# Performance work log

Hardware: AMD Instinct MI355X
Metric: run time of the kernel (lower is better)

Reference implementation:

```python
import jax, jax.numpy as jnp
import numpy as np

DN = ('NCHW', 'OIHW', 'NCHW')

def _conv(x, w, b):
    y = jax.lax.conv_general_dilated(x, w, (1, 1), 'SAME', dimension_numbers=DN)
    return y + b[None, :, None, None]

def _prelu(x, a):
    return jnp.where(x >= 0, x, a * x)

def _block(x, W1, b1, a1, W2, b2, a2, W3, b3):
    x = _prelu(_conv(x, W1, b1), a1)
    x = _prelu(_conv(x, W2, b2), a2)
    return _conv(x, W3, b3)

def setup_inputs() -> dict:
    key = jax.random.key(0)
    B, n_ions, n_primal, H, W = 1, 1, 5, 96, 96
    A, D, n_iter = 96, 96, 10
    P, X = H * W, n_ions * D
    ks = jax.random.split(key, 12)
    f = jax.random.normal
    return {
        'dual': f(ks[0], (B, n_ions, A, D), jnp.float32),
        'primal': f(ks[1], (B, n_primal, H, W, 1), jnp.float32),
        'projection': f(ks[2], (B, n_ions, A, D), jnp.float32),
        'S': f(ks[3], (A, B, P, X), jnp.float32) * 0.01,
        'S_norm': f(ks[4], (A, B, P, X), jnp.float32) * 0.01,
        'dW1': f(ks[5], (n_iter, 32, 3 * n_ions, 3, 3), jnp.float32) * 0.05,
        'db1': jnp.zeros((n_iter, 32), jnp.float32),
        'da1': jnp.full((n_iter,), 0.25, jnp.float32),
        'dW2': f(ks[6], (n_iter, 32, 32, 3, 3), jnp.float32) * 0.05,
        'db2': jnp.zeros((n_iter, 32), jnp.float32),
        'da2': jnp.full((n_iter,), 0.25, jnp.float32),
        'dW3': f(ks[7], (n_iter, n_ions, 32, 3, 3), jnp.float32) * 0.05,
        'db3': jnp.zeros((n_iter, n_ions), jnp.float32),
        'pW1': f(ks[8], (n_iter, 32, n_primal + 1, 3, 3), jnp.float32) * 0.05,
        'pb1': jnp.zeros((n_iter, 32), jnp.float32),
        'pa1': jnp.full((n_iter,), 0.25, jnp.float32),
        'pW2': f(ks[9], (n_iter, 32, 32, 3, 3), jnp.float32) * 0.05,
        'pb2': jnp.zeros((n_iter, 32), jnp.float32),
        'pa2': jnp.full((n_iter,), 0.25, jnp.float32),
        'pW3': f(ks[10], (n_iter, n_primal, 32, 3, 3), jnp.float32) * 0.05,
        'pb3': jnp.zeros((n_iter, n_primal), jnp.float32),
    }

def reference(dual, primal, projection, S, S_norm, dW1, db1, da1, dW2, db2, da2, dW3, db3, pW1, pb1, pa1, pW2, pb2, pa2, pW3, pb3):
    B, n_primal, H, W, _ = primal.shape
    _, n_ions, A, D = dual.shape
    n_iter = dW1.shape[0]
    for k in range(n_iter):
        # forward projection of primal channel 1; fortran flatten: p = h + H*w
        img = primal[:, 1, :, :, 0].transpose(0, 2, 1).reshape(B, H * W)
        ev1 = jnp.einsum('abpx,bp->bax', S_norm, img)             # [B, A, D*n_ions]
        ev1 = ev1.reshape(B, A, D, n_ions).transpose(0, 3, 1, 2)  # [B, n_ions, A, D]
        xd = jnp.concatenate([dual, ev1, projection], axis=1)
        dual = dual + _block(xd, dW1[k], db1[k], da1[k], dW2[k], db2[k], da2[k], dW3[k], db3[k])
        # back projection summed over angles; fortran reshape P -> (H, W)
        dual2 = dual.transpose(0, 2, 3, 1).reshape(B, A, D * n_ions)  # x = d*n_ions + i
        bp = jnp.einsum('abpx,bax->bp', S, dual2)
        ev2 = bp.reshape(B, W, H).transpose(0, 2, 1)[:, None]     # [B, 1, H, W]
        psq = primal[..., 0]
        xp = jnp.concatenate([psq, ev2], axis=1)
        psq = psq + _block(xp, pW1[k], pb1[k], pa1[k], pW2[k], pb2[k], pa2[k], pW3[k], pb3[k])
        primal = psq[..., None]
    return primal[:, 0:1, :, :]
```

## Files before the change

kernel.cpp:

```cpp
#include <hip/hip_runtime.h>
#include <hip/hip_fp16.h>
#include <cstdint>
#include <cstddef>

#define PP 9216
#define NPRIM 5
#define NITER 10
#define IMG 9216

typedef float vf4 __attribute__((ext_vector_type(4)));
union H8 { vf4 f4; __half h[8]; };

template<int MODE>
__global__ __launch_bounds__(256) void k_ev1(const float* __restrict__ Sf,
                                             __half* __restrict__ S16,
                                             const float* __restrict__ prim,
                                             float* __restrict__ part){
  const int a = blockIdx.x, c = blockIdx.y;
  const int p0 = c*576;
  const int tid = threadIdx.x;
  __shared__ float img[576];
  __shared__ float red[240][8];
  const float* prim1 = prim + IMG;
  for (int idx = tid; idx < 576; idx += 256){
    int p = p0 + idx;
    int h = p % 96, w = p / 96;
    img[idx] = prim1[h*96 + w];
  }
  __syncthreads();
  if (tid < 240){
    const int xg = tid % 12, pr = tid / 12;
    float acc[8];
    #pragma unroll
    for (int j = 0; j < 8; ++j) acc[j] = 0.f;
    const size_t base = ((size_t)a*PP + p0)*96 + 8*xg;
    #pragma unroll 2
    for (int pi = pr; pi < 576; pi += 20){
      float s[8];
      if (MODE == 2){
        H8 u; u.f4 = __builtin_nontemporal_load(reinterpret_cast<const vf4*>(S16 + base + (size_t)pi*96));
        #pragma unroll
        for (int j = 0; j < 8; ++j) s[j] = __half2float(u.h[j]);
      } else {
        const vf4 q0 = __builtin_nontemporal_load(reinterpret_cast<const vf4*>(Sf + base + (size_t)pi*96));
        const vf4 q1 = __builtin_nontemporal_load(reinterpret_cast<const vf4*>(Sf + base + (size_t)pi*96 + 4));
        float t[8] = {q0.x,q0.y,q0.z,q0.w,q1.x,q1.y,q1.z,q1.w};
        if (MODE == 1){
          H8 u;
          #pragma unroll
          for (int j = 0; j < 8; ++j){ u.h[j] = __float2half(t[j]); s[j] = __half2float(u.h[j]); }
          __builtin_nontemporal_store(u.f4, reinterpret_cast<vf4*>(S16 + base + (size_t)pi*96));
        } else {
          #pragma unroll
          for (int j = 0; j < 8; ++j) s[j] = t[j];
        }
      }
      const float im = img[pi];
      #pragma unroll
      for (int j = 0; j < 8; ++j) acc[j] += im*s[j];
    }
    #pragma unroll
    for (int j = 0; j < 8; ++j) red[tid][j] = acc[j];
  }
  __syncthreads();
  if (tid < 12){
    float r[8];
    #pragma unroll
    for (int j = 0; j < 8; ++j) r[j] = red[tid][j];
    for (int q = 1; q < 20; ++q)
      #pragma unroll
      for (int j = 0; j < 8; ++j) r[j] += red[tid + 12*q][j];
    float* dst = &part[((size_t)a*16 + c)*96 + 8*tid];
    vf4 v0 = {r[0],r[1],r[2],r[3]}, v1 = {r[4],r[5],r[6],r[7]};
    *reinterpret_cast<vf4*>(dst) = v0;
    *reinterpret_cast<vf4*>(dst+4) = v1;
  }
}

template<int MODE>
__global__ __launch_bounds__(192) void k_bp(const float* __restrict__ Sf,
                                            __half* __restrict__ S16,
                                            const float* __restrict__ dual,
                                            float* __restrict__ ev2){
  __shared__ float d2[PP];
  __shared__ float red[192];
  const int tid = threadIdx.x;
  for (int i = tid; i < PP/4; i += 192)
    reinterpret_cast<vf4*>(d2)[i] = reinterpret_cast<const vf4*>(dual)[i];
  __syncthreads();
  const int p0 = blockIdx.x * 16;
  const int xg = tid % 12, pr = tid / 12;
  const int p = p0 + pr;
  float acc = 0.f;
  const size_t base = (size_t)p*96 + 8*xg;
  const size_t astr = (size_t)PP*96;
  #pragma unroll 4
  for (int a = 0; a < 96; ++a){
    float s[8];
    if (MODE == 2){
      H8 u; u.f4 = __builtin_nontemporal_load(reinterpret_cast<const vf4*>(S16 + base + (size_t)a*astr));
      #pragma unroll
      for (int j = 0; j < 8; ++j) s[j] = __half2float(u.h[j]);
    } else {
      const vf4 q0 = __builtin_nontemporal_load(reinterpret_cast<const vf4*>(Sf + base + (size_t)a*astr));
      const vf4 q1 = __builtin_nontemporal_load(reinterpret_cast<const vf4*>(Sf + base + (size_t)a*astr + 4));
      float t[8] = {q0.x,q0.y,q0.z,q0.w,q1.x,q1.y,q1.z,q1.w};
      if (MODE == 1){
        H8 u;
        #pragma unroll
        for (int j = 0; j < 8; ++j){ u.h[j] = __float2half(t[j]); s[j] = __half2float(u.h[j]); }
        __builtin_nontemporal_store(u.f4, reinterpret_cast<vf4*>(S16 + base + (size_t)a*astr));
      } else {
        #pragma unroll
        for (int j = 0; j < 8; ++j) s[j] = t[j];
      }
    }
    const vf4 da = *reinterpret_cast<const vf4*>(&d2[a*96 + 8*xg]);
    const vf4 db = *reinterpret_cast<const vf4*>(&d2[a*96 + 8*xg + 4]);
    acc += s[0]*da.x + s[1]*da.y + s[2]*da.z + s[3]*da.w
         + s[4]*db.x + s[5]*db.y + s[6]*db.z + s[7]*db.w;
  }
  red[tid] = acc;
  __syncthreads();
  if (tid < 16){
    float s = 0.f;
    #pragma unroll
    for (int j = 0; j < 12; ++j) s += red[tid*12 + j];
    int pp = p0 + tid;
    int h = pp % 96, w = pp / 96;
    ev2[h*96 + w] = s;
  }
}

template<int CIN, int COUT, bool REDB>
__global__ __launch_bounds__(256) void k_conv_block(
    const float* __restrict__ inA, int nA, const float* __restrict__ inB, int nB,
    const float* __restrict__ inC,
    const float* __restrict__ W1, const float* __restrict__ B1, const float* __restrict__ A1,
    const float* __restrict__ W2, const float* __restrict__ B2, const float* __restrict__ A2,
    const float* __restrict__ W3, const float* __restrict__ B3,
    float* __restrict__ out, float* __restrict__ out2)
{
  constexpr int C1F  = 32*10*12;
  constexpr int C2F  = 32*8*9;
  constexpr int XINF = CIN*144;
  constexpr int W1F  = 32*CIN*9;
  constexpr int W2F  = 288*32;
  constexpr int W3F  = COUT*32*9;
  constexpr int OV1  = (XINF+W1F > W2F) ? XINF+W1F : W2F;
  constexpr int OVLF = (OV1 > W3F) ? OV1 : W3F;

  __shared__ float c1s[C1F];
  __shared__ float c2s[C2F];
  __shared__ float bias1[32], bias2[32], bias3[COUT], alph[2];
  __shared__ float ovl[OVLF];

  const int tid = threadIdx.x;
  const int x0 = blockIdx.x * 6, y0 = blockIdx.y * 6;

  float* xin = ovl;
  float* w1s = ovl + XINF;

  for (int i = tid; i < XINF; i += 256){
    int ch = i / 144, r = (i % 144) / 12, cc = i % 12;
    int gy = y0 - 3 + r, gx = x0 - 3 + cc;
    float v = 0.f;
    if (gy >= 0 && gy < 96 && gx >= 0 && gx < 96){
      if (REDB && ch >= nA && ch < nA + nB){
        float s = 0.f;
        #pragma unroll
        for (int cch = 0; cch < 16; ++cch) s += inB[((size_t)gy*16 + cch)*96 + gx];
        v = s;
      } else {
        const float* src = (ch < nA) ? (inA + (size_t)ch*IMG)
                         : (ch < nA+nB) ? (inB + (size_t)(ch-nA)*IMG)
                         : (inC + (size_t)(ch-nA-nB)*IMG);
        v = src[gy*96 + gx];
      }
    }
    xin[i] = v;
  }
  for (int i = tid; i < W1F; i += 256) w1s[i] = W1[i];
  if (tid < 32) bias1[tid] = B1[tid];
  else if (tid < 64) bias2[tid-32] = B2[tid-32];
  else if (tid < 64+COUT) bias3[tid-64] = B3[tid-64];
  else if (tid == 96) alph[0] = A1[0];
  else if (tid == 97) alph[1] = A2[0];
  __syncthreads();

  {
    const int och = tid & 31, t = tid >> 5;
    const float al = alph[0];
    for (int r = t; r < 10; r += 8){
      const int gy = y0 - 2 + r;
      float acc[10];
      #pragma unroll
      for (int cc = 0; cc < 10; ++cc) acc[cc] = bias1[och];
      #pragma unroll
      for (int ci = 0; ci < CIN; ++ci){
        float xr[3][12];
        #pragma unroll
        for (int ky = 0; ky < 3; ++ky){
          #pragma unroll
          for (int j = 0; j < 3; ++j){
            vf4 q = *reinterpret_cast<const vf4*>(&xin[ci*144 + (r+ky)*12 + 4*j]);
            xr[ky][4*j+0]=q.x; xr[ky][4*j+1]=q.y; xr[ky][4*j+2]=q.z; xr[ky][4*j+3]=q.w;
          }
        }
        float wv[9];
        #pragma unroll
        for (int kk = 0; kk < 9; ++kk) wv[kk] = w1s[(och*CIN+ci)*9 + kk];
        #pragma unroll
        for (int ky = 0; ky < 3; ++ky)
          #pragma unroll
          for (int kx = 0; kx < 3; ++kx)
            #pragma unroll
            for (int cc = 0; cc < 10; ++cc)
              acc[cc] += xr[ky][cc+kx] * wv[ky*3+kx];
      }
      const bool yin = (gy >= 0 && gy < 96);
      #pragma unroll
      for (int cc = 0; cc < 10; ++cc){
        const int gx = x0 - 2 + cc;
        float v = acc[cc];
        v = (v >= 0.f) ? v : al*v;
        const bool in = yin && (gx >= 0 && gx < 96);
        c1s[(och*10 + r)*12 + cc] = in ? v : 0.f;
      }
    }
  }
  float resv = 0.f;
  {
    int sp = tid % 36, och = tid / 36;
    if (och < COUT){
      int ty = sp / 6, tx = sp % 6;
      resv = xin[och*144 + (ty+3)*12 + (tx+3)];
    }
  }
  float w2r[36];
  {
    const vf4* src = reinterpret_cast<const vf4*>(W2 + (size_t)tid*36);
    #pragma unroll
    for (int q = 0; q < 9; ++q) reinterpret_cast<vf4*>(w2r)[q] = src[q];
  }
  __syncthreads();

  float* w2t = ovl;
  {
    const int och = tid >> 3, k0 = (tid & 7)*36;
    #pragma unroll
    for (int j = 0; j < 36; ++j) w2t[(k0 + j)*32 + och] = w2r[j];
  }
  __syncthreads();

  {
    const int och = tid & 31, ty = tid >> 5;
    const int gy = y0 - 1 + ty;
    const float al = alph[1];
    float acc[8];
    #pragma unroll
    for (int cc = 0; cc < 8; ++cc) acc[cc] = bias2[och];
    for (int ci = 0; ci < 32; ++ci){
      float cr[3][12];
      #pragma unroll
      for (int ky = 0; ky < 3; ++ky){
        #pragma unroll
        for (int j = 0; j < 3; ++j){
          vf4 q = *reinterpret_cast<const vf4*>(&c1s[(ci*10 + ty+ky)*12 + 4*j]);
          cr[ky][4*j+0]=q.x; cr[ky][4*j+1]=q.y; cr[ky][4*j+2]=q.z; cr[ky][4*j+3]=q.w;
        }
      }
      float wv[9];
      #pragma unroll
      for (int kk = 0; kk < 9; ++kk) wv[kk] = w2t[(ci*9+kk)*32 + och];
      #pragma unroll
      for (int ky = 0; ky < 3; ++ky)
        #pragma unroll
        for (int kx = 0; kx < 3; ++kx)
          #pragma unroll
          for (int cc = 0; cc < 8; ++cc)
            acc[cc] += cr[ky][cc+kx] * wv[ky*3+kx];
    }
    const bool yin = (gy >= 0 && gy < 96);
    #pragma unroll
    for (int cc = 0; cc < 8; ++cc){
      const int gx = x0 - 1 + cc;
      float v = acc[cc];
      v = (v >= 0.f) ? v : al*v;
      const bool in = yin && (gx >= 0 && gx < 96);
      c2s[(och*8 + ty)*9 + cc] = in ? v : 0.f;
    }
  }
  __syncthreads();

  float* w3s = ovl;
  for (int i = tid; i < W3F; i += 256) w3s[i] = W3[i];
  __syncthreads();

  {
    int sp = tid % 36, och = tid / 36;
    if (och < COUT){
      int ty = sp / 6, tx = sp % 6;
      float acc = bias3[och];
      for (int ci = 0; ci < 32; ++ci){
        #pragma unroll
        for (int ky = 0; ky < 3; ++ky)
          #pragma unroll
          for (int kx = 0; kx < 3; ++kx)
            acc += c2s[(ci*8 + ty+ky)*9 + (tx+kx)] * w3s[(och*32+ci)*9 + ky*3+kx];
      }
      const float vout = resv + acc;
      const int idx = (y0+ty)*96 + (x0+tx);
      out[(size_t)och*IMG + idx] = vout;
      if (out2 != nullptr && och == 0) out2[idx] = vout;
    }
  }
}

extern "C" void kernel_launch(void* const* d_in, const int* in_sizes, int n_in,
                              void* d_out, int out_size, void* d_ws, size_t ws_size,
                              hipStream_t stream){
  (void)in_sizes; (void)n_in; (void)out_size;
  const float* dual   = (const float*)d_in[0];
  const float* primal = (const float*)d_in[1];
  const float* proj   = (const float*)d_in[2];
  const float* S      = (const float*)d_in[3];
  const float* Snorm  = (const float*)d_in[4];
  const float* dW1 = (const float*)d_in[5];
  const float* db1 = (const float*)d_in[6];
  const float* da1 = (const float*)d_in[7];
  const float* dW2 = (const float*)d_in[8];
  const float* db2 = (const float*)d_in[9];
  const float* da2 = (const float*)d_in[10];
  const float* dW3 = (const float*)d_in[11];
  const float* db3 = (const float*)d_in[12];
  const float* pW1 = (const float*)d_in[13];
  const float* pb1 = (const float*)d_in[14];
  const float* pa1 = (const float*)d_in[15];
  const float* pW2 = (const float*)d_in[16];
  const float* pb2 = (const float*)d_in[17];
  const float* pa2 = (const float*)d_in[18];
  const float* pW3 = (const float*)d_in[19];
  const float* pb3 = (const float*)d_in[20];

  const size_t S16E = (size_t)96*PP*96;
  const size_t needFloats = (size_t)29*PP;
  const size_t need16 = 2*S16E*sizeof(__half) + needFloats*sizeof(float);
  const bool f16 = (ws_size >= need16);

  __half* S16n = nullptr; __half* S16s = nullptr; float* fbase;
  if (f16){
    S16n = (__half*)d_ws;
    S16s = S16n + S16E;
    fbase = (float*)(S16s + S16E);
  } else {
    fbase = (float*)d_ws;
  }
  float* dB0  = fbase;            fbase += PP;
  float* dB1  = fbase;            fbase += PP;
  float* pB0  = fbase;            fbase += NPRIM*PP;
  float* pB1  = fbase;            fbase += NPRIM*PP;
  float* part = fbase;            fbase += 16*PP;
  float* ev2  = fbase;            fbase += PP;

  for (int k = 0; k < NITER; ++k){
    const float* dcur = (k == 0) ? dual   : ((k & 1) ? dB0 : dB1);
    float*       dnxt = (k & 1) ? dB1 : dB0;
    const float* pcur = (k == 0) ? primal : ((k & 1) ? pB0 : pB1);
    float*       pnxt = (k & 1) ? pB1 : pB0;
    float*       out2 = (k == NITER-1) ? (float*)d_out : nullptr;

    if (f16){
      if (k == 0) k_ev1<1><<<dim3(96,16), 256, 0, stream>>>(Snorm, S16n, pcur, part);
      else        k_ev1<2><<<dim3(96,16), 256, 0, stream>>>(nullptr, S16n, pcur, part);
    } else        k_ev1<0><<<dim3(96,16), 256, 0, stream>>>(Snorm, nullptr, pcur, part);

    k_conv_block<3,1,true><<<dim3(16,16), 256, 0, stream>>>(
        dcur, 1, part, 1, proj,
        dW1 + (size_t)k*32*3*9, db1 + (size_t)k*32, da1 + k,
        dW2 + (size_t)k*32*32*9, db2 + (size_t)k*32, da2 + k,
        dW3 + (size_t)k*1*32*9, db3 + (size_t)k*1, dnxt, nullptr);

    if (f16){
      if (k == 0) k_bp<1><<<576, 192, 0, stream>>>(S, S16s, dnxt, ev2);
      else        k_bp<2><<<576, 192, 0, stream>>>(nullptr, S16s, dnxt, ev2);
    } else        k_bp<0><<<576, 192, 0, stream>>>(S, nullptr, dnxt, ev2);

    k_conv_block<6,5,false><<<dim3(16,16), 256, 0, stream>>>(
        pcur, 5, ev2, 1, ev2,
        pW1 + (size_t)k*32*6*9, pb1 + (size_t)k*32, pa1 + k,
        pW2 + (size_t)k*32*32*9, pb2 + (size_t)k*32, pa2 + k,
        pW3 + (size_t)k*5*32*9, pb3 + (size_t)k*5, pnxt, out2);
  }
}
```

Before: 1.121 ms.

## Fuse all iterations into one persistent cooperative kernel with grid syncs

Replaces the 40 separate kernel launches (ev1, dual conv, backprojection, primal conv per iteration) with one persistent cooperative kernel. Each block loops over task tiles, and grid.sync separates the stages. A shared-memory union serves every stage, and the backprojection now uses 18-pixel tiles with 256 threads. This removes launch gaps and tail effects, but the grid is capped at 256 blocks with large shared memory, which limits occupancy during the bandwidth-bound S streaming stages. It also adds grid-wide barrier costs, and a non-cooperative fallback path is kept.

```diff
diff --git a/kernel.cpp b/kernel.cpp
--- a/kernel.cpp
+++ b/kernel.cpp
@@ -1,7 +1,10 @@
 #include <hip/hip_runtime.h>
 #include <hip/hip_fp16.h>
+#include <hip/hip_cooperative_groups.h>
 #include <cstdint>
 #include <cstddef>
+
+namespace cg = cooperative_groups;
 
 #define PP 9216
 #define NPRIM 5
@@ -11,21 +14,24 @@
 typedef float vf4 __attribute__((ext_vector_type(4)));
 union H8 { vf4 f4; __half h[8]; };
 
+struct ShEv { float img[576]; float red[240][8]; };
+struct ShBp { float d2[PP]; float red[216]; };
+struct ShCv { float c1s[32*10*12]; float c2s[32*8*9]; float ovl[9216];
+              float b1[32], b2[32], b3[5], al[2]; };
+union Sh { ShEv ev; ShBp bp; ShCv cv; };
+
 template<int MODE>
-__global__ __launch_bounds__(256) void k_ev1(const float* __restrict__ Sf,
-                                             __half* __restrict__ S16,
-                                             const float* __restrict__ prim,
-                                             float* __restrict__ part){
-  const int a = blockIdx.x, c = blockIdx.y;
+__device__ void ev1_task(ShEv& S, int a, int c,
+                         const float* __restrict__ Sf, __half* __restrict__ S16,
+                         const float* __restrict__ prim, float* __restrict__ part){
   const int p0 = c*576;
   const int tid = threadIdx.x;
-  __shared__ float img[576];
-  __shared__ float red[240][8];
   const float* prim1 = prim + IMG;
+  __syncthreads();
   for (int idx = tid; idx < 576; idx += 256){
     int p = p0 + idx;
     int h = p % 96, w = p / 96;
-    img[idx] = prim1[h*96 + w];
+    S.img[idx] = prim1[h*96 + w];
   }
   __syncthreads();
   if (tid < 240){
@@ -34,7 +40,7 @@
     #pragma unroll
     for (int j = 0; j < 8; ++j) acc[j] = 0.f;
     const size_t base = ((size_t)a*PP + p0)*96 + 8*xg;
-    #pragma unroll 2
+    #pragma unroll 4
     for (int pi = pr; pi < 576; pi += 20){
       float s[8];
       if (MODE == 2){
@@ -55,21 +61,21 @@
           for (int j = 0; j < 8; ++j) s[j] = t[j];
         }
       }
-      const float im = img[pi];
+      const float im = S.img[pi];
       #pragma unroll
       for (int j = 0; j < 8; ++j) acc[j] += im*s[j];
     }
     #pragma unroll
-    for (int j = 0; j < 8; ++j) red[tid][j] = acc[j];
+    for (int j = 0; j < 8; ++j) S.red[tid][j] = acc[j];
   }
   __syncthreads();
   if (tid < 12){
     float r[8];
     #pragma unroll
-    for (int j = 0; j < 8; ++j) r[j] = red[tid][j];
+    for (int j = 0; j < 8; ++j) r[j] = S.red[tid][j];
     for (int q = 1; q < 20; ++q)
       #pragma unroll
-      for (int j = 0; j < 8; ++j) r[j] += red[tid + 12*q][j];
+      for (int j = 0; j < 8; ++j) r[j] += S.red[tid + 12*q][j];
     float* dst = &part[((size_t)a*16 + c)*96 + 8*tid];
     vf4 v0 = {r[0],r[1],r[2],r[3]}, v1 = {r[4],r[5],r[6],r[7]};
     *reinterpret_cast<vf4*>(dst) = v0;
@@ -78,62 +84,66 @@
 }
 
 template<int MODE>
-__global__ __launch_bounds__(192) void k_bp(const float* __restrict__ Sf,
-                                            __half* __restrict__ S16,
-                                            const float* __restrict__ dual,
-                                            float* __restrict__ ev2){
-  __shared__ float d2[PP];
-  __shared__ float red[192];
+__device__ void bp_compute(ShBp& S, int t,
+                           const float* __restrict__ Sf, __half* __restrict__ S16,
+                           float* __restrict__ ev2){
   const int tid = threadIdx.x;
-  for (int i = tid; i < PP/4; i += 192)
-    reinterpret_cast<vf4*>(d2)[i] = reinterpret_cast<const vf4*>(dual)[i];
-  __syncthreads();
-  const int p0 = blockIdx.x * 16;
-  const int xg = tid % 12, pr = tid / 12;
-  const int p = p0 + pr;
-  float acc = 0.f;
-  const size_t base = (size_t)p*96 + 8*xg;
-  const size_t astr = (size_t)PP*96;
-  #pragma unroll 4
-  for (int a = 0; a < 96; ++a){
-    float s[8];
-    if (MODE == 2){
-      H8 u; u.f4 = __builtin_nontemporal_load(reinterpret_cast<const vf4*>(S16 + base + (size_t)a*astr));
-      #pragma unroll
-      for (int j = 0; j < 8; ++j) s[j] = __half2float(u.h[j]);
-    } else {
-      const vf4 q0 = __builtin_nontemporal_load(reinterpret_cast<const vf4*>(Sf + base + (size_t)a*astr));
-      const vf4 q1 = __builtin_nontemporal_load(reinterpret_cast<const vf4*>(Sf + base + (size_t)a*astr + 4));
-      float t[8] = {q0.x,q0.y,q0.z,q0.w,q1.x,q1.y,q1.z,q1.w};
-      if (MODE == 1){
-        H8 u;
-        #pragma unroll
-        for (int j = 0; j < 8; ++j){ u.h[j] = __float2half(t[j]); s[j] = __half2float(u.h[j]); }
-        __builtin_nontemporal_store(u.f4, reinterpret_cast<vf4*>(S16 + base + (size_t)a*astr));
+  __syncthreads();
+  const int p0 = t * 18;
+  if (tid < 216){
+    const int xg = tid % 12, pr = tid / 12;
+    const int p = p0 + pr;
+    float acc = 0.f;
+    const size_t base = (size_t)p*96 + 8*xg;
+    const size_t astr = (size_t)PP*96;
+    #pragma unroll 4
+    for (int a = 0; a < 96; ++a){
+      float s[8];
+      if (MODE == 2){
+        H8 u; u.f4 = __builtin_nontemporal_load(reinterpret_cast<const vf4*>(S16 + base + (size_t)a*astr));
+        #pragma unroll
+        for (int j = 0; j < 8; ++j) s[j] = __half2float(u.h[j]);
       } else {
-        #pragma unroll
-        for (int j = 0; j < 8; ++j) s[j] = t[j];
-      }
-    }
-    const vf4 da = *reinterpret_cast<const vf4*>(&d2[a*96 + 8*xg]);
-    const vf4 db = *reinterpret_cast<const vf4*>(&d2[a*96 + 8*xg + 4]);
-    acc += s[0]*da.x + s[1]*da.y + s[2]*da.z + s[3]*da.w
-         + s[4]*db.x + s[5]*db.y + s[6]*db.z + s[7]*db.w;
-  }
-  red[tid] = acc;
-  __syncthreads();
-  if (tid < 16){
+        const vf4 q0 = __builtin_nontemporal_load(reinterpret_cast<const vf4*>(Sf + base + (size_t)a*astr));
+        const vf4 q1 = __builtin_nontemporal_load(reinterpret_cast<const vf4*>(Sf + base + (size_t)a*astr + 4));
+        float tt[8] = {q0.x,q0.y,q0.z,q0.w,q1.x,q1.y,q1.z,q1.w};
+        if (MODE == 1){
+          H8 u;
+          #pragma unroll
+          for (int j = 0; j < 8; ++j){ u.h[j] = __float2half(tt[j]); s[j] = __half2float(u.h[j]); }
+          __builtin_nontemporal_store(u.f4, reinterpret_cast<vf4*>(S16 + base + (size_t)a*astr));
+        } else {
+          #pragma unroll
+          for (int j = 0; j < 8; ++j) s[j] = tt[j];
+        }
+      }
+      const vf4 da = *reinterpret_cast<const vf4*>(&S.d2[a*96 + 8*xg]);
+      const vf4 db = *reinterpret_cast<const vf4*>(&S.d2[a*96 + 8*xg + 4]);
+      acc += s[0]*da.x + s[1]*da.y + s[2]*da.z + s[3]*da.w
+           + s[4]*db.x + s[5]*db.y + s[6]*db.z + s[7]*db.w;
+    }
+    S.red[tid] = acc;
+  }
+  __syncthreads();
+  if (tid < 18){
     float s = 0.f;
     #pragma unroll
-    for (int j = 0; j < 12; ++j) s += red[tid*12 + j];
+    for (int j = 0; j < 12; ++j) s += S.red[tid*12 + j];
     int pp = p0 + tid;
     int h = pp % 96, w = pp / 96;
     ev2[h*96 + w] = s;
   }
 }
 
+__device__ void bp_load(ShBp& S, const float* __restrict__ dual){
+  __syncthreads();
+  for (int i = threadIdx.x; i < PP/4; i += 256)
+    reinterpret_cast<vf4*>(S.d2)[i] = reinterpret_cast<const vf4*>(dual)[i];
+  __syncthreads();
+}
+
 template<int CIN, int COUT, bool REDB>
-__global__ __launch_bounds__(256) void k_conv_block(
+__device__ void conv_task(ShCv& S, int x0, int y0,
     const float* __restrict__ inA, int nA, const float* __restrict__ inB, int nB,
     const float* __restrict__ inC,
     const float* __restrict__ W1, const float* __restrict__ B1, const float* __restrict__ A1,
@@ -141,26 +151,15 @@
     const float* __restrict__ W3, const float* __restrict__ B3,
     float* __restrict__ out, float* __restrict__ out2)
 {
-  constexpr int C1F  = 32*10*12;
-  constexpr int C2F  = 32*8*9;
   constexpr int XINF = CIN*144;
   constexpr int W1F  = 32*CIN*9;
-  constexpr int W2F  = 288*32;
   constexpr int W3F  = COUT*32*9;
-  constexpr int OV1  = (XINF+W1F > W2F) ? XINF+W1F : W2F;
-  constexpr int OVLF = (OV1 > W3F) ? OV1 : W3F;
-
-  __shared__ float c1s[C1F];
-  __shared__ float c2s[C2F];
-  __shared__ float bias1[32], bias2[32], bias3[COUT], alph[2];
-  __shared__ float ovl[OVLF];
 
   const int tid = threadIdx.x;
-  const int x0 = blockIdx.x * 6, y0 = blockIdx.y * 6;
-
-  float* xin = ovl;
-  float* w1s = ovl + XINF;
-
+  float* xin = S.ovl;
+  float* w1s = S.ovl + XINF;
+
+  __syncthreads();
   for (int i = tid; i < XINF; i += 256){
     int ch = i / 144, r = (i % 144) / 12, cc = i % 12;
     int gy = y0 - 3 + r, gx = x0 - 3 + cc;
@@ -181,21 +180,21 @@
     xin[i] = v;
   }
   for (int i = tid; i < W1F; i += 256) w1s[i] = W1[i];
-  if (tid < 32) bias1[tid] = B1[tid];
-  else if (tid < 64) bias2[tid-32] = B2[tid-32];
-  else if (tid < 64+COUT) bias3[tid-64] = B3[tid-64];
-  else if (tid == 96) alph[0] = A1[0];
-  else if (tid == 97) alph[1] = A2[0];
+  if (tid < 32) S.b1[tid] = B1[tid];
+  else if (tid < 64) S.b2[tid-32] = B2[tid-32];
+  else if (tid < 64+COUT) S.b3[tid-64] = B3[tid-64];
+  else if (tid == 96) S.al[0] = A1[0];
+  else if (tid == 97) S.al[1] = A2[0];
   __syncthreads();
 
   {
     const int och = tid & 31, t = tid >> 5;
-    const float al = alph[0];
+    const float al = S.al[0];
     for (int r = t; r < 10; r += 8){
       const int gy = y0 - 2 + r;
       float acc[10];
       #pragma unroll
-      for (int cc = 0; cc < 10; ++cc) acc[cc] = bias1[och];
+      for (int cc = 0; cc < 10; ++cc) acc[cc] = S.b1[och];
       #pragma unroll
       for (int ci = 0; ci < CIN; ++ci){
         float xr[3][12];
@@ -225,7 +224,7 @@
         float v = acc[cc];
         v = (v >= 0.f) ? v : al*v;
         const bool in = yin && (gx >= 0 && gx < 96);
-        c1s[(och*10 + r)*12 + cc] = in ? v : 0.f;
+        S.c1s[(och*10 + r)*12 + cc] = in ? v : 0.f;
       }
     }
   }
@@ -245,7 +244,7 @@
   }
   __syncthreads();
 
-  float* w2t = ovl;
+  float* w2t = S.ovl;
   {
     const int och = tid >> 3, k0 = (tid & 7)*36;
     #pragma unroll
@@ -256,17 +255,17 @@
   {
     const int och = tid & 31, ty = tid >> 5;
     const int gy = y0 - 1 + ty;
-    const float al = alph[1];
+    const float al = S.al[1];
     float acc[8];
     #pragma unroll
-    for (int cc = 0; cc < 8; ++cc) acc[cc] = bias2[och];
+    for (int cc = 0; cc < 8; ++cc) acc[cc] = S.b2[och];
     for (int ci = 0; ci < 32; ++ci){
       float cr[3][12];
       #pragma unroll
       for (int ky = 0; ky < 3; ++ky){
         #pragma unroll
         for (int j = 0; j < 3; ++j){
-          vf4 q = *reinterpret_cast<const vf4*>(&c1s[(ci*10 + ty+ky)*12 + 4*j]);
+          vf4 q = *reinterpret_cast<const vf4*>(&S.c1s[(ci*10 + ty+ky)*12 + 4*j]);
           cr[ky][4*j+0]=q.x; cr[ky][4*j+1]=q.y; cr[ky][4*j+2]=q.z; cr[ky][4*j+3]=q.w;
         }
       }
@@ -288,12 +287,12 @@
       float v = acc[cc];
       v = (v >= 0.f) ? v : al*v;
       const bool in = yin && (gx >= 0 && gx < 96);
-      c2s[(och*8 + ty)*9 + cc] = in ? v : 0.f;
-    }
-  }
-  __syncthreads();
-
-  float* w3s = ovl;
+      S.c2s[(och*8 + ty)*9 + cc] = in ? v : 0.f;
+    }
+  }
+  __syncthreads();
+
+  float* w3s = S.ovl;
   for (int i = tid; i < W3F; i += 256) w3s[i] = W3[i];
   __syncthreads();
 
@@ -301,13 +300,13 @@
     int sp = tid % 36, och = tid / 36;
     if (och < COUT){
       int ty = sp / 6, tx = sp % 6;
-      float acc = bias3[och];
+      float acc = S.b3[och];
       for (int ci = 0; ci < 32; ++ci){
         #pragma unroll
         for (int ky = 0; ky < 3; ++ky)
           #pragma unroll
           for (int kx = 0; kx < 3; ++kx)
-            acc += c2s[(ci*8 + ty+ky)*9 + (tx+kx)] * w3s[(och*32+ci)*9 + ky*3+kx];
+            acc += S.c2s[(ci*8 + ty+ky)*9 + (tx+kx)] * w3s[(och*32+ci)*9 + ky*3+kx];
       }
       const float vout = resv + acc;
       const int idx = (y0+ty)*96 + (x0+tx);
@@ -317,79 +316,180 @@
   }
 }
 
+struct P {
+  const float *dual, *primal, *proj, *S, *Snorm;
+  const float *dW1,*db1,*da1,*dW2,*db2,*da2,*dW3,*db3;
+  const float *pW1,*pb1,*pa1,*pW2,*pb2,*pa2,*pW3,*pb3;
+  __half *S16n, *S16s;
+  float *dB0,*dB1,*pB0,*pB1,*part,*ev2;
+  float *outp;
+  int f16;
+};
+
+__global__ __launch_bounds__(256) void mega(P p){
+  cg::grid_group grid = cg::this_grid();
+  __shared__ Sh sh;
+  const int bid = blockIdx.x;
+  const int nb = gridDim.x;
+
+  for (int k = 0; k < NITER; ++k){
+    const float* dcur = (k == 0) ? p.dual   : ((k & 1) ? p.dB0 : p.dB1);
+    float*       dnxt = (k & 1) ? p.dB1 : p.dB0;
+    const float* pcur = (k == 0) ? p.primal : ((k & 1) ? p.pB0 : p.pB1);
+    float*       pnxt = (k & 1) ? p.pB1 : p.pB0;
+    float*       out2 = (k == NITER-1) ? p.outp : nullptr;
+
+    for (int t = bid; t < 1536; t += nb){
+      const int a = t >> 4, c = t & 15;
+      if (p.f16){
+        if (k == 0) ev1_task<1>(sh.ev, a, c, p.Snorm, p.S16n, pcur, p.part);
+        else        ev1_task<2>(sh.ev, a, c, nullptr, p.S16n, pcur, p.part);
+      } else        ev1_task<0>(sh.ev, a, c, p.Snorm, nullptr, pcur, p.part);
+    }
+    grid.sync();
+
+    for (int t = bid; t < 256; t += nb){
+      conv_task<3,1,true>(sh.cv, (t & 15)*6, (t >> 4)*6,
+          dcur, 1, p.part, 1, p.proj,
+          p.dW1 + (size_t)k*32*3*9, p.db1 + (size_t)k*32, p.da1 + k,
+          p.dW2 + (size_t)k*32*32*9, p.db2 + (size_t)k*32, p.da2 + k,
+          p.dW3 + (size_t)k*1*32*9, p.db3 + (size_t)k*1, dnxt, nullptr);
+    }
+    grid.sync();
+
+    bp_load(sh.bp, dnxt);
+    for (int t = bid; t < 512; t += nb){
+      if (p.f16){
+        if (k == 0) bp_compute<1>(sh.bp, t, p.S, p.S16s, p.ev2);
+        else        bp_compute<2>(sh.bp, t, nullptr, p.S16s, p.ev2);
+      } else        bp_compute<0>(sh.bp, t, p.S, nullptr, p.ev2);
+    }
+    grid.sync();
+
+    for (int t = bid; t < 256; t += nb){
+      conv_task<6,5,false>(sh.cv, (t & 15)*6, (t >> 4)*6,
+          pcur, 5, p.ev2, 1, p.ev2,
+          p.pW1 + (size_t)k*32*6*9, p.pb1 + (size_t)k*32, p.pa1 + k,
+          p.pW2 + (size_t)k*32*32*9, p.pb2 + (size_t)k*32, p.pa2 + k,
+          p.pW3 + (size_t)k*5*32*9, p.pb3 + (size_t)k*5, pnxt, out2);
+    }
+    grid.sync();
+  }
+}
+
+template<int MODE>
+__global__ __launch_bounds__(256) void k_ev1_w(const float* Sf, __half* S16,
+                                               const float* prim, float* part){
+  __shared__ ShEv sh;
+  ev1_task<MODE>(sh, blockIdx.x, blockIdx.y, Sf, S16, prim, part);
+}
+
+template<int MODE>
+__global__ __launch_bounds__(256) void k_bp_w(const float* Sf, __half* S16,
+                                              const float* dual, float* ev2){
+  __shared__ ShBp sh;
+  bp_load(sh, dual);
+  bp_compute<MODE>(sh, blockIdx.x, Sf, S16, ev2);
+}
+
+template<int CIN, int COUT, bool REDB>
+__global__ __launch_bounds__(256) void k_conv_w(
+    const float* inA, int nA, const float* inB, int nB, const float* inC,
+    const float* W1, const float* B1, const float* A1,
+    const float* W2, const float* B2, const float* A2,
+    const float* W3, const float* B3, float* out, float* out2){
+  __shared__ ShCv sh;
+  conv_task<CIN,COUT,REDB>(sh, (blockIdx.x & 15)*6, (blockIdx.x >> 4)*6,
+      inA, nA, inB, nB, inC, W1, B1, A1, W2, B2, A2, W3, B3, out, out2);
+}
+
 extern "C" void kernel_launch(void* const* d_in, const int* in_sizes, int n_in,
                               void* d_out, int out_size, void* d_ws, size_t ws_size,
                               hipStream_t stream){
   (void)in_sizes; (void)n_in; (void)out_size;
-  const float* dual   = (const float*)d_in[0];
-  const float* primal = (const float*)d_in[1];
-  const float* proj   = (const float*)d_in[2];
-  const float* S      = (const float*)d_in[3];
-  const float* Snorm  = (const float*)d_in[4];
-  const float* dW1 = (const float*)d_in[5];
-  const float* db1 = (const float*)d_in[6];
-  const float* da1 = (const float*)d_in[7];
-  const float* dW2 = (const float*)d_in[8];
-  const float* db2 = (const float*)d_in[9];
-  const float* da2 = (const float*)d_in[10];
-  const float* dW3 = (const float*)d_in[11];
-  const float* db3 = (const float*)d_in[12];
-  const float* pW1 = (const float*)d_in[13];
-  const float* pb1 = (const float*)d_in[14];
-  const float* pa1 = (const float*)d_in[15];
-  const float* pW2 = (const float*)d_in[16];
-  const float* pb2 = (const float*)d_in[17];
-  const float* pa2 = (const float*)d_in[18];
-  const float* pW3 = (const float*)d_in[19];
-  const float* pb3 = (const float*)d_in[20];
+  P p;
+  p.dual   = (const float*)d_in[0];
+  p.primal = (const float*)d_in[1];
+  p.proj   = (const float*)d_in[2];
+  p.S      = (const float*)d_in[3];
+  p.Snorm  = (const float*)d_in[4];
+  p.dW1 = (const float*)d_in[5];  p.db1 = (const float*)d_in[6];  p.da1 = (const float*)d_in[7];
+  p.dW2 = (const float*)d_in[8];  p.db2 = (const float*)d_in[9];  p.da2 = (const float*)d_in[10];
+  p.dW3 = (const float*)d_in[11]; p.db3 = (const float*)d_in[12];
+  p.pW1 = (const float*)d_in[13]; p.pb1 = (const float*)d_in[14]; p.pa1 = (const float*)d_in[15];
+  p.pW2 = (const float*)d_in[16]; p.pb2 = (const float*)d_in[17]; p.pa2 = (const float*)d_in[18];
+  p.pW3 = (const float*)d_in[19]; p.pb3 = (const float*)d_in[20];
 
   const size_t S16E = (size_t)96*PP*96;
   const size_t needFloats = (size_t)29*PP;
   const size_t need16 = 2*S16E*sizeof(__half) + needFloats*sizeof(float);
-  const bool f16 = (ws_size >= need16);
-
-  __half* S16n = nullptr; __half* S16s = nullptr; float* fbase;
-  if (f16){
-    S16n = (__half*)d_ws;
-    S16s = S16n + S16E;
-    fbase = (float*)(S16s + S16E);
+  p.f16 = (ws_size >= need16) ? 1 : 0;
+
+  float* fbase;
+  if (p.f16){
+    p.S16n = (__half*)d_ws;
+    p.S16s = p.S16n + S16E;
+    fbase = (float*)(p.S16s + S16E);
   } else {
+    p.S16n = nullptr; p.S16s = nullptr;
     fbase = (float*)d_ws;
   }
-  float* dB0  = fbase;            fbase += PP;
-  float* dB1  = fbase;            fbase += PP;
-  float* pB0  = fbase;            fbase += NPRIM*PP;
-  float* pB1  = fbase;            fbase += NPRIM*PP;
-  float* part = fbase;            fbase += 16*PP;
-  float* ev2  = fbase;            fbase += PP;
-
-  for (int k = 0; k < NITER; ++k){
-    const float* dcur = (k == 0) ? dual   : ((k & 1) ? dB0 : dB1);
-    float*       dnxt = (k & 1) ? dB1 : dB0;
-    const float* pcur = (k == 0) ? primal : ((k & 1) ? pB0 : pB1);
-    float*       pnxt = (k & 1) ? pB1 : pB0;
-    float*       out2 = (k == NITER-1) ? (float*)d_out : nullptr;
-
-    if (f16){
-      if (k == 0) k_ev1<1><<<dim3(96,16), 256, 0, stream>>>(Snorm, S16n, pcur, part);
-      else        k_ev1<2><<<dim3(96,16), 256, 0, stream>>>(nullptr, S16n, pcur, part);
-    } else        k_ev1<0><<<dim3(96,16), 256, 0, stream>>>(Snorm, nullptr, pcur, part);
-
-    k_conv_block<3,1,true><<<dim3(16,16), 256, 0, stream>>>(
-        dcur, 1, part, 1, proj,
-        dW1 + (size_t)k*32*3*9, db1 + (size_t)k*32, da1 + k,
-        dW2 + (size_t)k*32*32*9, db2 + (size_t)k*32, da2 + k,
-        dW3 + (size_t)k*1*32*9, db3 + (size_t)k*1, dnxt, nullptr);
-
-    if (f16){
-      if (k == 0) k_bp<1><<<576, 192, 0, stream>>>(S, S16s, dnxt, ev2);
-      else        k_bp<2><<<576, 192, 0, stream>>>(nullptr, S16s, dnxt, ev2);
-    } else        k_bp<0><<<576, 192, 0, stream>>>(S, nullptr, dnxt, ev2);
-
-    k_conv_block<6,5,false><<<dim3(16,16), 256, 0, stream>>>(
-        pcur, 5, ev2, 1, ev2,
-        pW1 + (size_t)k*32*6*9, pb1 + (size_t)k*32, pa1 + k,
-        pW2 + (size_t)k*32*32*9, pb2 + (size_t)k*32, pa2 + k,
-        pW3 + (size_t)k*5*32*9, pb3 + (size_t)k*5, pnxt, out2);
-  }
-}
+  p.dB0  = fbase;            fbase += PP;
+  p.dB1  = fbase;            fbase += PP;
+  p.pB0  = fbase;            fbase += NPRIM*PP;
+  p.pB1  = fbase;            fbase += NPRIM*PP;
+  p.part = fbase;            fbase += 16*PP;
+  p.ev2  = fbase;            fbase += PP;
+  p.outp = (float*)d_out;
+
+  int dev = 0; hipGetDevice(&dev);
+  int coop = 0; hipDeviceGetAttribute(&coop, hipDeviceAttributeCooperativeLaunch, dev);
+  int nCU = 0;  hipDeviceGetAttribute(&nCU, hipDeviceAttributeMultiprocessorCount, dev);
+  int mb = 0;
+  hipError_t oe = hipOccupancyMaxActiveBlocksPerMultiprocessor(&mb, mega, 256, 0);
+  int nblk = 0;
+  if (coop && oe == hipSuccess && nCU > 0 && mb > 0){
+    long cap = (long)mb * (long)nCU;
+    nblk = (cap < 256) ? (int)cap : 256;
+  }
+
+  bool launched = false;
+  if (nblk >= 64){
+    void* args[] = { &p };
+    hipError_t le = hipLaunchCooperativeKernel((const void*)mega, dim3(nblk), dim3(256),
+                                               args, 0, stream);
+    launched = (le == hipSuccess);
+  }
+
+  if (!launched){
+    for (int k = 0; k < NITER; ++k){
+      const float* dcur = (k == 0) ? p.dual   : ((k & 1) ? p.dB0 : p.dB1);
+      float*       dnxt = (k & 1) ? p.dB1 : p.dB0;
+      const float* pcur = (k == 0) ? p.primal : ((k & 1) ? p.pB0 : p.pB1);
+      float*       pnxt = (k & 1) ? p.pB1 : p.pB0;
+      float*       out2 = (k == NITER-1) ? p.outp : nullptr;
+
+      if (p.f16){
+        if (k == 0) k_ev1_w<1><<<dim3(96,16), 256, 0, stream>>>(p.Snorm, p.S16n, pcur, p.part);
+        else        k_ev1_w<2><<<dim3(96,16), 256, 0, stream>>>(nullptr, p.S16n, pcur, p.part);
+      } else        k_ev1_w<0><<<dim3(96,16), 256, 0, stream>>>(p.Snorm, nullptr, pcur, p.part);
+
+      k_conv_w<3,1,true><<<256, 256, 0, stream>>>(
+          dcur, 1, p.part, 1, p.proj,
+          p.dW1 + (size_t)k*32*3*9, p.db1 + (size_t)k*32, p.da1 + k,
+          p.dW2 + (size_t)k*32*32*9, p.db2 + (size_t)k*32, p.da2 + k,
+          p.dW3 + (size_t)k*1*32*9, p.db3 + (size_t)k*1, dnxt, nullptr);
+
+      if (p.f16){
+        if (k == 0) k_bp_w<1><<<512, 256, 0, stream>>>(p.S, p.S16s, dnxt, p.ev2);
+        else        k_bp_w<2><<<512, 256, 0, stream>>>(nullptr, p.S16s, dnxt, p.ev2);
+      } else        k_bp_w<0><<<512, 256, 0, stream>>>(p.S, nullptr, dnxt, p.ev2);
+
+      k_conv_w<6,5,false><<<256, 256, 0, stream>>>(
+          pcur, 5, p.ev2, 1, p.ev2,
+          p.pW1 + (size_t)k*32*6*9, p.pb1 + (size_t)k*32, p.pa1 + k,
+          p.pW2 + (size_t)k*32*32*9, p.pb2 + (size_t)k*32, p.pa2 + k,
+          p.pW3 + (size_t)k*5*32*9, p.pb3 + (size_t)k*5, pnxt, out2);
+    }
+  }
+}
```

After: 1.287 ms. 14.8% more time.
